# Kernel tuning notes

Measured on AMD Instinct MI355X. Metric: run time of the kernel, lower is better.

## Reference

```python
import jax, jax.numpy as jnp
import numpy as np

TEMPERATURE = 0.07
UNIFORMITY_THRESHOLD = 0.1
SEPARATION_MARGIN = 2.0
W_SUPCON = 1.0
W_SEPARATION = 0.5
W_UNIFORMITY = 0.5
NUM_MASKS = 6


def setup_inputs() -> dict:
    key = jax.random.key(0)
    k1, k2, k3 = jax.random.split(key, 3)
    B, H, Wd, D = 16, 33, 33, 512
    emb = jax.random.normal(k1, (B, H, Wd, D), dtype=jnp.float32)
    emb = emb / jnp.linalg.norm(emb, axis=-1, keepdims=True)  # module expects normalized embeddings
    masks = jax.random.uniform(k2, (B, NUM_MASKS, H, Wd), dtype=jnp.float32)
    is_forged = jax.random.uniform(k3, (B,), dtype=jnp.float32)
    return {"embeddings": emb, "masks": masks, "is_forged": is_forged}


def _labels(masks):
    # masks: (M, H, W). Channel i writes label i+1 where mask>0.5 (if channel has any mass);
    # later channels overwrite earlier -> equivalent to max over active hits.
    active = masks.sum(axis=(1, 2)) > 0  # (M,)
    hit = (masks > 0.5) & active[:, None, None]
    ids = jnp.arange(1, masks.shape[0] + 1)[:, None, None]
    return jnp.max(jnp.where(hit, ids, 0), axis=0).reshape(-1)  # (H*W,)


def _per_image(emb, masks, forged):
    H, W, D = emb.shape
    feat = emb.reshape(-1, D)  # (N, D)
    N = feat.shape[0]
    labels = _labels(masks)  # (N,) in 0..M
    L = masks.shape[0] + 1  # possible labels 0..6
    onehot = (labels[:, None] == jnp.arange(L)[None, :]).astype(feat.dtype)  # (N, L)
    cnt = onehot.sum(axis=0)  # (L,)
    sums = onehot.T @ feat  # (L, D) per-label sums
    mean_l = sums / jnp.maximum(cnt, 1.0)[:, None]  # safe per-label centroids

    # ---- SupCon (PixelSupConLoss) ----
    logits = (feat @ feat.T) / TEMPERATURE  # (N, N)
    logits = logits - jax.lax.stop_gradient(logits.max(axis=1, keepdims=True))
    same = (labels[:, None] == labels[None, :]).astype(feat.dtype)
    logits_mask = 1.0 - jnp.eye(N, dtype=feat.dtype)
    pos = same * logits_mask
    exp_l = jnp.exp(logits) * logits_mask
    log_prob = logits - jnp.log(exp_l.sum(axis=1, keepdims=True) + 1e-6)
    pos_sum = pos.sum(axis=1)
    mean_lp = (pos * log_prob).sum(axis=1) / jnp.where(pos_sum == 0, 1.0, pos_sum)
    anchor_valid = (pos_sum > 0).astype(feat.dtype)
    n_anchor = anchor_valid.sum()
    supcon = (-mean_lp * anchor_valid).sum() / jnp.maximum(n_anchor, 1.0)
    supcon_valid = n_anchor > 0

    # ---- Inter-instance separation ----
    present = cnt > 0
    cn = (mean_l ** 2).sum(axis=1)  # (L,)
    sq = cn[:, None] + cn[None, :] - 2.0 * (mean_l @ mean_l.T)  # squared centroid dists
    tri = jnp.triu(jnp.ones((L, L), dtype=bool), k=1)
    pair_valid = tri & present[:, None] & present[None, :]
    d = jnp.sqrt(jnp.where(pair_valid, jnp.maximum(sq, 0.0), 1.0))
    terms = jnp.where(pair_valid, jax.nn.relu(SEPARATION_MARGIN - d), 0.0)
    n_pairs = pair_valid.sum().astype(feat.dtype)
    sep = terms.sum() / jnp.maximum(n_pairs, 1.0)
    sep_valid = present.sum() >= 2

    # ---- Uniformity ----
    rn2 = (feat ** 2).sum(axis=1)  # (N,)
    q_l = onehot.T @ rn2  # (L,) per-label sum of squared norms
    var_l = q_l / jnp.maximum(cnt, 1.0) - (mean_l ** 2).sum(axis=1)  # E||e||^2 - ||mean||^2
    lbl_valid = (cnt >= 2) & (var_l > UNIFORMITY_THRESHOLD)
    inst_loss = jnp.where(lbl_valid, var_l - UNIFORMITY_THRESHOLD, 0.0).sum()
    n_lbl = lbl_valid.sum().astype(feat.dtype)
    uni_forged = inst_loss / jnp.maximum(n_lbl, 1.0)
    uni_forged_valid = n_lbl > 0
    mean_all = feat.mean(axis=0)
    var_all = ((feat - mean_all) ** 2).sum(axis=1).mean()
    uni_unf = jnp.where(var_all > UNIFORMITY_THRESHOLD, var_all - UNIFORMITY_THRESHOLD, 0.0)
    uni_unf_valid = var_all > UNIFORMITY_THRESHOLD

    is_f = forged >= 0.5
    uni = jnp.where(is_f, uni_forged, uni_unf)
    uni_valid = jnp.where(is_f, uni_forged_valid, uni_unf_valid)
    return supcon, supcon_valid, sep, sep_valid, uni, uni_valid


def _agg(vals, valids):
    v = valids.astype(vals.dtype)
    n = v.sum()
    return jnp.where(n > 0, (vals * v).sum() / jnp.maximum(n, 1.0), 0.0)


def reference(embeddings, masks, is_forged):
    sc, scv, sp, spv, un, unv = jax.vmap(_per_image)(embeddings, masks, is_forged)
    supcon = _agg(sc, scv)
    separation = _agg(sp, spv)
    uniformity = _agg(un, unv)
    return W_SUPCON * supcon + W_SEPARATION * separation + W_UNIFORMITY * uniformity
```

## Files before the change

### kernel.cpp

```cpp
#include <hip/hip_runtime.h>
#include <math.h>

#define NPIX 1089
#define DIM 512
#define NIMG 16
#define NLBL 8
#define NMASK 6
#define INVT 14.2857142857142857f

#define NGRP 72
#define NROWPAD 1152
#define NT9 9


typedef short v8s __attribute__((ext_vector_type(8)));
typedef float v4f __attribute__((ext_vector_type(4)));

__device__ __forceinline__ float wave_reduce(float x) {
#pragma unroll
  for (int o = 32; o > 0; o >>= 1) x += __shfl_xor(x, o, 64);
  return x;
}
__device__ __forceinline__ unsigned bfbits(float x) {
  unsigned u = __float_as_uint(x);
  return (u + 0x7FFFu + ((u >> 16) & 1u)) >> 16;
}
__device__ __forceinline__ unsigned pk(float lo, float hi) {
  return bfbits(lo) | (bfbits(hi) << 16);
}

__global__ __launch_bounds__(512) void k_packsum(const float* __restrict__ emb,
                                                 const float* __restrict__ masks,
                                                 uint2* __restrict__ bfemb2,
                                                 float* __restrict__ sums9,
                                                 int* __restrict__ labels,
                                                 float* __restrict__ cnt9,
                                                 unsigned* __restrict__ counter) {
  int b = blockIdx.y;
  int g9 = blockIdx.x >> 1, dh = blockIdx.x & 1;
  int tid = threadIdx.x, dd = tid & 63, w4 = tid >> 6, lane = tid & 63;
  __shared__ float msum[NMASK];
  __shared__ int slab[128];
  __shared__ int scnt[NLBL];
  __shared__ float4 red[8 * 8 * 64];
  if (tid < NMASK) msum[tid] = 0.f;
  if (tid < NLBL) scnt[tid] = 0;
  if (b == 0 && blockIdx.x == 0 && tid == 0) *counter = 0u;
  __syncthreads();
  {
    float am[NMASK] = {0.f, 0.f, 0.f, 0.f, 0.f, 0.f};
    for (int p = tid; p < NPIX; p += 512) {
#pragma unroll
      for (int c = 0; c < NMASK; c++) am[c] += masks[((size_t)b * NMASK + c) * NPIX + p];
    }
#pragma unroll
    for (int c = 0; c < NMASK; c++) {
      float v = wave_reduce(am[c]);
      if (lane == 0) atomicAdd(&msum[c], v);
    }
  }
  __syncthreads();
  if (tid < 128) {
    int r = g9 * 128 + tid;
    int lab = 7;
    if (r < NPIX) {
      lab = 0;
#pragma unroll
      for (int c = 0; c < NMASK; c++) {
        float mv = masks[((size_t)b * NMASK + c) * NPIX + r];
        if (mv > 0.5f && msum[c] > 0.f) lab = c + 1;
      }
    }
    slab[tid] = lab;
    if (dh == 0) {
      labels[b * NROWPAD + r] = lab;
      if (r < NPIX) atomicAdd(&scnt[lab], 1);
    }
  }
  __syncthreads();
  if (dh == 0 && tid < NLBL) cnt9[((size_t)b * NT9 + g9) * NLBL + tid] = (float)scnt[tid];
  float4 fa0 = {0,0,0,0}, fa1 = {0,0,0,0}, fa2 = {0,0,0,0}, fa3 = {0,0,0,0};
  float4 fa4 = {0,0,0,0}, fa5 = {0,0,0,0}, fa6 = {0,0,0,0}, fa7 = {0,0,0,0};
  int kc = dh * 8 + (dd >> 3), q = (dd >> 1) & 3, half = dd & 1;
#pragma unroll
  for (int k = 0; k < 16; k++) {
    int r = g9 * 128 + w4 + k * 8;
    bool v = r < NPIX;
    int rc = v ? r : (NPIX - 1);
    float4 x = ((const float4*)(emb + (size_t)(b * NPIX + rc) * DIM))[dh * 64 + dd];
    if (!v) x = make_float4(0.f, 0.f, 0.f, 0.f);
    uint2 o = make_uint2(pk(x.x, x.y), pk(x.z, x.w));
    bfemb2[((((size_t)(b * NGRP + (r >> 4)) * 16 + kc) * 64) + q * 16 + (r & 15)) * 2 + half] = o;
    int lab = __builtin_amdgcn_readfirstlane(slab[r - g9 * 128]);
    switch (lab) {
      case 0: fa0.x += x.x; fa0.y += x.y; fa0.z += x.z; fa0.w += x.w; break;
      case 1: fa1.x += x.x; fa1.y += x.y; fa1.z += x.z; fa1.w += x.w; break;
      case 2: fa2.x += x.x; fa2.y += x.y; fa2.z += x.z; fa2.w += x.w; break;
      case 3: fa3.x += x.x; fa3.y += x.y; fa3.z += x.z; fa3.w += x.w; break;
      case 4: fa4.x += x.x; fa4.y += x.y; fa4.z += x.z; fa4.w += x.w; break;
      case 5: fa5.x += x.x; fa5.y += x.y; fa5.z += x.z; fa5.w += x.w; break;
      case 6: fa6.x += x.x; fa6.y += x.y; fa6.z += x.z; fa6.w += x.w; break;
      default: fa7.x += x.x; fa7.y += x.y; fa7.z += x.z; fa7.w += x.w; break;
    }
  }
  red[(0 * 8 + w4) * 64 + dd] = fa0; red[(1 * 8 + w4) * 64 + dd] = fa1;
  red[(2 * 8 + w4) * 64 + dd] = fa2; red[(3 * 8 + w4) * 64 + dd] = fa3;
  red[(4 * 8 + w4) * 64 + dd] = fa4; red[(5 * 8 + w4) * 64 + dd] = fa5;
  red[(6 * 8 + w4) * 64 + dd] = fa6; red[(7 * 8 + w4) * 64 + dd] = fa7;
  __syncthreads();
  int l = tid >> 6, d2 = tid & 63;
  float4 s = {0,0,0,0};
#pragma unroll
  for (int ww = 0; ww < 8; ww++) {
    float4 t = red[(l * 8 + ww) * 64 + d2];
    s.x += t.x; s.y += t.y; s.z += t.z; s.w += t.w;
  }
  *(float4*)&sums9[(((size_t)(b * NT9 + g9) * NLBL + l) * DIM) + dh * 256 + d2 * 4] = s;
}

__global__ __launch_bounds__(512) void k_epass6(const uint4* __restrict__ bfemb4,
                                                float* __restrict__ E9) {
  int n = blockIdx.x;
  int img = ((n & 7) << 1) | ((n >> 3) & 1);
  int t = n >> 4;
  int it = 0, rem = t;
  while (rem >= NT9 - it) { rem -= NT9 - it; it++; }
  int jt = it + rem;
  int i0 = it * 128, j0 = jt * 128;
  bool diag = (it == jt);
  int tid = threadIdx.x, lane = tid & 63, w = tid >> 6;
  int wm = w >> 2, wn = w & 3;
  int quad = lane >> 4, l15 = lane & 15;
  __shared__ uint4 st[2][2][8][64];
  __shared__ float Ered[4][128];
  __shared__ float Ecol[2][128];

  size_t gA = ((size_t)(img * NGRP + it * 8 + w) * 16) * 64 + lane;
  size_t gB = ((size_t)(img * NGRP + jt * 8 + w) * 16) * 64 + lane;
  int bsel = diag ? 0 : 1;

#define STAGE(kc, buf)                                                          \
  {                                                                             \
    __builtin_amdgcn_global_load_lds(                                           \
        (const __attribute__((address_space(1))) void*)(bfemb4 + gA + (kc) * 64), \
        (__attribute__((address_space(3))) void*)&st[buf][0][w][0], 16, 0, 0);  \
    if (!diag)                                                                  \
      __builtin_amdgcn_global_load_lds(                                         \
          (const __attribute__((address_space(1))) void*)(bfemb4 + gB + (kc) * 64), \
          (__attribute__((address_space(3))) void*)&st[buf][1][w][0], 16, 0, 0); \
  }

  v4f acc[4][2];
#pragma unroll
  for (int mf = 0; mf < 4; mf++)
#pragma unroll
    for (int nf = 0; nf < 2; nf++) acc[mf][nf] = (v4f){0.f, 0.f, 0.f, 0.f};

  STAGE(0, 0);
  __syncthreads();
#pragma unroll
  for (int kc = 0; kc < 16; kc++) {
    int cur = kc & 1;
    if (kc < 15) STAGE(kc + 1, cur ^ 1);
    v8s a[4], b[2];
#pragma unroll
    for (int f = 0; f < 4; f++) a[f] = *(const v8s*)&st[cur][0][wm * 4 + f][lane];
#pragma unroll
    for (int f = 0; f < 2; f++) b[f] = *(const v8s*)&st[cur][bsel][wn * 2 + f][lane];
#pragma unroll
    for (int mf = 0; mf < 4; mf++)
#pragma unroll
      for (int nf = 0; nf < 2; nf++)
        acc[mf][nf] = __builtin_amdgcn_mfma_f32_16x16x32_bf16(a[mf], b[nf],
                                                              acc[mf][nf], 0, 0, 0);
    __syncthreads();
  }
#undef STAGE

  float scol[2] = {0.f, 0.f};
#pragma unroll
  for (int mf = 0; mf < 4; mf++) {
#pragma unroll
    for (int rr = 0; rr < 4; rr++) {
      int i = i0 + wm * 64 + mf * 16 + quad * 4 + rr;
      float srow = 0.f;
#pragma unroll
      for (int nf = 0; nf < 2; nf++) {
        int j = j0 + wn * 32 + nf * 16 + l15;
        float e = __expf((acc[mf][nf][rr] - 1.f) * INVT);
        bool ok = (j < NPIX) && (!diag || (i != j && i < NPIX));
        e = ok ? e : 0.f;
        srow += e;
        scol[nf] += e;
      }
      srow += __shfl_xor(srow, 1); srow += __shfl_xor(srow, 2);
      srow += __shfl_xor(srow, 4); srow += __shfl_xor(srow, 8);
      if (l15 == 0) Ered[wn][wm * 64 + mf * 16 + quad * 4 + rr] = srow;
    }
  }
  if (!diag) {
#pragma unroll
    for (int nf = 0; nf < 2; nf++) {
      float s = scol[nf];
      s += __shfl_xor(s, 16); s += __shfl_xor(s, 32);
      if (quad == 0) Ecol[wm][wn * 32 + nf * 16 + l15] = s;
    }
  }
  __syncthreads();
  if (tid < 128) {
    E9[((size_t)img * NT9 + jt) * NROWPAD + i0 + tid] =
        Ered[0][tid] + Ered[1][tid] + Ered[2][tid] + Ered[3][tid];
    if (!diag)
      E9[((size_t)img * NT9 + it) * NROWPAD + j0 + tid] = Ecol[0][tid] + Ecol[1][tid];
  }
}

__global__ __launch_bounds__(512) void k_imgfinal(const float* __restrict__ sums9,
                                                  const int* __restrict__ labels,
                                                  const float* __restrict__ cnt9,
                                                  const float* __restrict__ E9,
                                                  const float* __restrict__ is_forged,
                                                  unsigned* __restrict__ counter,
                                                  float* __restrict__ per_img,
                                                  float* __restrict__ out) {
  int b = blockIdx.x, tid = threadIdx.x;
  int wave = tid >> 6, lane = tid & 63;
  __shared__ float ssum[NLBL * DIM];
  __shared__ float sCnt[NLBL], sR[NLBL][NLBL];
  __shared__ float sLog, sNA;
  if (tid < NLBL) {
    float s = 0.f;
#pragma unroll
    for (int g = 0; g < NT9; g++) s += cnt9[((size_t)b * NT9 + g) * NLBL + tid];
    sCnt[tid] = s;
  }
  if (tid == 0) { sLog = 0.f; sNA = 0.f; }
  for (int o = tid; o < NLBL * DIM; o += 512) {
    float s = 0.f;
#pragma unroll
    for (int g = 0; g < NT9; g++) s += sums9[((size_t)(b * NT9 + g) * NLBL * DIM) + o];
    ssum[o] = s;
  }
  __syncthreads();
  float ll = 0.f, na = 0.f;
  for (int p = tid; p < NPIX; p += 512) {
    int lab = labels[b * NROWPAD + p];
    if (sCnt[lab] >= 1.5f) {
      float e = 0.f;
#pragma unroll
      for (int s = 0; s < NT9; s++) e += E9[((size_t)b * NT9 + s) * NROWPAD + p];
      ll += __logf(e + 1e-6f);
      na += 1.f;
    }
  }
  ll = wave_reduce(ll); na = wave_reduce(na);
  if (lane == 0) { atomicAdd(&sLog, ll); atomicAdd(&sNA, na); }
  for (int t = wave; t < 36; t += 8) {
    int a = 0, tt = t;
    while (tt >= NLBL - a) { tt -= NLBL - a; a++; }
    int bb = a + tt;
    float d0 = 0.f;
    for (int k = lane; k < DIM; k += 64) d0 += ssum[a * DIM + k] * ssum[bb * DIM + k];
    d0 = wave_reduce(d0);
    if (lane == 0) sR[a][bb] = d0;
  }
  __syncthreads();
  if (tid == 0) {
    float spos = 0.f;
    for (int l = 0; l < NLBL; l++) {
      float c = sCnt[l];
      if (c >= 1.5f) spos += (sR[l][l] - c) * INVT / (c - 1.f) - c * INVT;
    }
    float nA = sNA;
    float sc = nA > 0.f ? (sLog - spos) / nA : 0.f;
    float scv = nA > 0.f ? 1.f : 0.f;
    float inv[NLBL]; int present[NLBL]; int nPres = 0;
    for (int l = 0; l < NLBL; l++) {
      present[l] = sCnt[l] > 0.f;
      nPres += present[l];
      inv[l] = 1.f / fmaxf(sCnt[l], 1.f);
    }
    float sepsum = 0.f; int npairs = 0;
    for (int a = 0; a < NLBL; a++)
      for (int c = a + 1; c < NLBL; c++)
        if (present[a] && present[c]) {
          float sq_ = sR[a][a] * inv[a] * inv[a] + sR[c][c] * inv[c] * inv[c]
                    - 2.f * sR[a][c] * inv[a] * inv[c];
          float dd = sqrtf(fmaxf(sq_, 0.f));
          sepsum += fmaxf(2.f - dd, 0.f);
          npairs++;
        }
    float sep = npairs > 0 ? sepsum / (float)npairs : 0.f;
    float sepv = nPres >= 2 ? 1.f : 0.f;
    float inst = 0.f; int nlbl = 0;
    for (int l = 0; l < NLBL; l++) {
      float var = 1.f - sR[l][l] * inv[l] * inv[l];
      if (sCnt[l] >= 2.f && var > 0.1f) { inst += var - 0.1f; nlbl++; }
    }
    float unif = nlbl > 0 ? inst / (float)nlbl : 0.f;
    float unifv = nlbl > 0 ? 1.f : 0.f;
    float tot2 = 0.f;
    for (int a = 0; a < NLBL; a++) {
      tot2 += sR[a][a];
      for (int c = a + 1; c < NLBL; c++) tot2 += 2.f * sR[a][c];
    }
    float Nf = (float)NPIX;
    float var_all = 1.f - tot2 / (Nf * Nf);
    float uniu = var_all > 0.1f ? var_all - 0.1f : 0.f;
    float uniuv = var_all > 0.1f ? 1.f : 0.f;
    bool isf = is_forged[b] >= 0.5f;
    per_img[b * 6 + 0] = sc;
    per_img[b * 6 + 1] = scv;
    per_img[b * 6 + 2] = sep;
    per_img[b * 6 + 3] = sepv;
    per_img[b * 6 + 4] = isf ? unif : uniu;
    per_img[b * 6 + 5] = isf ? unifv : uniuv;
    __threadfence();
    unsigned tk = atomicAdd(counter, 1u);
    if (tk == NIMG - 1) {
      __threadfence();
      float accv[3] = {0.f, 0.f, 0.f}, accn[3] = {0.f, 0.f, 0.f};
      for (int bb = 0; bb < NIMG; bb++)
        for (int m = 0; m < 3; m++) {
          float v = per_img[bb * 6 + m * 2], val = per_img[bb * 6 + m * 2 + 1];
          accv[m] += v * val; accn[m] += val;
        }
      float scA = accn[0] > 0.f ? accv[0] / accn[0] : 0.f;
      float sepA = accn[1] > 0.f ? accv[1] / accn[1] : 0.f;
      float uniA = accn[2] > 0.f ? accv[2] / accn[2] : 0.f;
      out[0] = 1.0f * scA + 0.5f * sepA + 0.5f * uniA;
    }
  }
}

extern "C" void kernel_launch(void* const* d_in, const int* in_sizes, int n_in,
                              void* d_out, int out_size, void* d_ws, size_t ws_size,
                              hipStream_t stream) {
  const float* emb = (const float*)d_in[0];
  const float* masks = (const float*)d_in[1];
  const float* isf = (const float*)d_in[2];
  float* out = (float*)d_out;
  char* ws = (char*)d_ws;
  size_t off = 0;
  uint4* bfemb4 = (uint4*)(ws + off);
  off += (size_t)NIMG * NGRP * 16 * 64 * 16;
  float* E9 = (float*)(ws + off);     off += sizeof(float) * NIMG * NT9 * NROWPAD;
  float* sums9 = (float*)(ws + off);  off += sizeof(float) * NIMG * NT9 * NLBL * DIM;
  int* labels = (int*)(ws + off);     off += sizeof(int) * NIMG * NROWPAD;
  float* cnt9 = (float*)(ws + off);   off += sizeof(float) * NIMG * NT9 * NLBL;
  float* per_img = (float*)(ws + off); off += sizeof(float) * NIMG * 6;
  off = (off + 127) & ~(size_t)127;
  unsigned* counter = (unsigned*)(ws + off); off += 128;

  k_packsum<<<dim3(18, NIMG), 512, 0, stream>>>(emb, masks, (uint2*)bfemb4, sums9,
                                                labels, cnt9, counter);
  k_epass6<<<45 * NIMG, 512, 0, stream>>>(bfemb4, E9);
  k_imgfinal<<<NIMG, 512, 0, stream>>>(sums9, labels, cnt9, E9, isf, counter, per_img, out);
}
```

Baseline: 123.2 us.

## Fuse per-image finalization into Gram tile kernel via last-block atomic counters

Removes the separate k_imgfinal launch. Each tile block of the E-pass kernel now increments a per-image atomic counter, and the last of that image's 45 tiles runs the per-image reduction, reusing the staging LDS for label sums. A second counter picks the last image to write the scalar output. This saves a kernel launch and lets finalization of early images overlap with tiles still running for other images, at the cost of extra shared memory and a serialized tail in one block per image.

```diff
diff --git a/kernel.cpp b/kernel.cpp
--- a/kernel.cpp
+++ b/kernel.cpp
@@ -35,7 +35,7 @@
                                                  float* __restrict__ sums9,
                                                  int* __restrict__ labels,
                                                  float* __restrict__ cnt9,
-                                                 unsigned* __restrict__ counter) {
+                                                 unsigned* __restrict__ counters) {
   int b = blockIdx.y;
   int g9 = blockIdx.x >> 1, dh = blockIdx.x & 1;
   int tid = threadIdx.x, dd = tid & 63, w4 = tid >> 6, lane = tid & 63;
@@ -45,7 +45,7 @@
   __shared__ float4 red[8 * 8 * 64];
   if (tid < NMASK) msum[tid] = 0.f;
   if (tid < NLBL) scnt[tid] = 0;
-  if (b == 0 && blockIdx.x == 0 && tid == 0) *counter = 0u;
+  if (b == 0 && blockIdx.x == 0 && tid < 32) counters[tid] = 0u;
   __syncthreads();
   {
     float am[NMASK] = {0.f, 0.f, 0.f, 0.f, 0.f, 0.f};
@@ -118,8 +118,15 @@
   *(float4*)&sums9[(((size_t)(b * NT9 + g9) * NLBL + l) * DIM) + dh * 256 + d2 * 4] = s;
 }
 
-__global__ __launch_bounds__(512) void k_epass6(const uint4* __restrict__ bfemb4,
-                                                float* __restrict__ E9) {
+__global__ __launch_bounds__(512) void k_epass7(const uint4* __restrict__ bfemb4,
+                                                float* __restrict__ E9,
+                                                const float* __restrict__ sums9,
+                                                const int* __restrict__ labels,
+                                                const float* __restrict__ cnt9,
+                                                const float* __restrict__ is_forged,
+                                                unsigned* __restrict__ counters,
+                                                float* __restrict__ per_img,
+                                                float* __restrict__ out) {
   int n = blockIdx.x;
   int img = ((n & 7) << 1) | ((n >> 3) & 1);
   int t = n >> 4;
@@ -134,6 +141,9 @@
   __shared__ uint4 st[2][2][8][64];
   __shared__ float Ered[4][128];
   __shared__ float Ecol[2][128];
+  __shared__ float sCnt[NLBL], sR[NLBL][NLBL];
+  __shared__ float sLog, sNA;
+  __shared__ int sflag;
 
   size_t gA = ((size_t)(img * NGRP + it * 8 + w) * 16) * 64 + lane;
   size_t gB = ((size_t)(img * NGRP + jt * 8 + w) * 16) * 64 + lane;
@@ -213,122 +223,121 @@
     if (!diag)
       E9[((size_t)img * NT9 + it) * NROWPAD + j0 + tid] = Ecol[0][tid] + Ecol[1][tid];
   }
-}
-
-__global__ __launch_bounds__(512) void k_imgfinal(const float* __restrict__ sums9,
-                                                  const int* __restrict__ labels,
-                                                  const float* __restrict__ cnt9,
-                                                  const float* __restrict__ E9,
-                                                  const float* __restrict__ is_forged,
-                                                  unsigned* __restrict__ counter,
-                                                  float* __restrict__ per_img,
-                                                  float* __restrict__ out) {
-  int b = blockIdx.x, tid = threadIdx.x;
-  int wave = tid >> 6, lane = tid & 63;
-  __shared__ float ssum[NLBL * DIM];
-  __shared__ float sCnt[NLBL], sR[NLBL][NLBL];
-  __shared__ float sLog, sNA;
-  if (tid < NLBL) {
-    float s = 0.f;
-#pragma unroll
-    for (int g = 0; g < NT9; g++) s += cnt9[((size_t)b * NT9 + g) * NLBL + tid];
-    sCnt[tid] = s;
-  }
-  if (tid == 0) { sLog = 0.f; sNA = 0.f; }
-  for (int o = tid; o < NLBL * DIM; o += 512) {
-    float s = 0.f;
-#pragma unroll
-    for (int g = 0; g < NT9; g++) s += sums9[((size_t)(b * NT9 + g) * NLBL * DIM) + o];
-    ssum[o] = s;
-  }
-  __syncthreads();
-  float ll = 0.f, na = 0.f;
-  for (int p = tid; p < NPIX; p += 512) {
-    int lab = labels[b * NROWPAD + p];
-    if (sCnt[lab] >= 1.5f) {
-      float e = 0.f;
-#pragma unroll
-      for (int s = 0; s < NT9; s++) e += E9[((size_t)b * NT9 + s) * NROWPAD + p];
-      ll += __logf(e + 1e-6f);
-      na += 1.f;
-    }
-  }
-  ll = wave_reduce(ll); na = wave_reduce(na);
-  if (lane == 0) { atomicAdd(&sLog, ll); atomicAdd(&sNA, na); }
-  for (int t = wave; t < 36; t += 8) {
-    int a = 0, tt = t;
-    while (tt >= NLBL - a) { tt -= NLBL - a; a++; }
-    int bb = a + tt;
-    float d0 = 0.f;
-    for (int k = lane; k < DIM; k += 64) d0 += ssum[a * DIM + k] * ssum[bb * DIM + k];
-    d0 = wave_reduce(d0);
-    if (lane == 0) sR[a][bb] = d0;
-  }
   __syncthreads();
   if (tid == 0) {
-    float spos = 0.f;
-    for (int l = 0; l < NLBL; l++) {
-      float c = sCnt[l];
-      if (c >= 1.5f) spos += (sR[l][l] - c) * INVT / (c - 1.f) - c * INVT;
-    }
-    float nA = sNA;
-    float sc = nA > 0.f ? (sLog - spos) / nA : 0.f;
-    float scv = nA > 0.f ? 1.f : 0.f;
-    float inv[NLBL]; int present[NLBL]; int nPres = 0;
-    for (int l = 0; l < NLBL; l++) {
-      present[l] = sCnt[l] > 0.f;
-      nPres += present[l];
-      inv[l] = 1.f / fmaxf(sCnt[l], 1.f);
-    }
-    float sepsum = 0.f; int npairs = 0;
-    for (int a = 0; a < NLBL; a++)
-      for (int c = a + 1; c < NLBL; c++)
-        if (present[a] && present[c]) {
-          float sq_ = sR[a][a] * inv[a] * inv[a] + sR[c][c] * inv[c] * inv[c]
-                    - 2.f * sR[a][c] * inv[a] * inv[c];
-          float dd = sqrtf(fmaxf(sq_, 0.f));
-          sepsum += fmaxf(2.f - dd, 0.f);
-          npairs++;
-        }
-    float sep = npairs > 0 ? sepsum / (float)npairs : 0.f;
-    float sepv = nPres >= 2 ? 1.f : 0.f;
-    float inst = 0.f; int nlbl = 0;
-    for (int l = 0; l < NLBL; l++) {
-      float var = 1.f - sR[l][l] * inv[l] * inv[l];
-      if (sCnt[l] >= 2.f && var > 0.1f) { inst += var - 0.1f; nlbl++; }
-    }
-    float unif = nlbl > 0 ? inst / (float)nlbl : 0.f;
-    float unifv = nlbl > 0 ? 1.f : 0.f;
-    float tot2 = 0.f;
-    for (int a = 0; a < NLBL; a++) {
-      tot2 += sR[a][a];
-      for (int c = a + 1; c < NLBL; c++) tot2 += 2.f * sR[a][c];
-    }
-    float Nf = (float)NPIX;
-    float var_all = 1.f - tot2 / (Nf * Nf);
-    float uniu = var_all > 0.1f ? var_all - 0.1f : 0.f;
-    float uniuv = var_all > 0.1f ? 1.f : 0.f;
-    bool isf = is_forged[b] >= 0.5f;
-    per_img[b * 6 + 0] = sc;
-    per_img[b * 6 + 1] = scv;
-    per_img[b * 6 + 2] = sep;
-    per_img[b * 6 + 3] = sepv;
-    per_img[b * 6 + 4] = isf ? unif : uniu;
-    per_img[b * 6 + 5] = isf ? unifv : uniuv;
     __threadfence();
-    unsigned tk = atomicAdd(counter, 1u);
-    if (tk == NIMG - 1) {
+    unsigned tk = atomicAdd(&counters[img], 1u);
+    sflag = (tk == 44u) ? 1 : 0;
+  }
+  __syncthreads();
+  if (!sflag) return;
+  __threadfence();
+
+  {
+    int b = img;
+    float* ssum = (float*)&st[0][0][0][0];
+    if (tid < NLBL) {
+      float s = 0.f;
+#pragma unroll
+      for (int g = 0; g < NT9; g++) s += cnt9[((size_t)b * NT9 + g) * NLBL + tid];
+      sCnt[tid] = s;
+    }
+    if (tid == 0) { sLog = 0.f; sNA = 0.f; }
+    for (int o = tid; o < NLBL * DIM; o += 512) {
+      float s = 0.f;
+#pragma unroll
+      for (int g = 0; g < NT9; g++) s += sums9[((size_t)(b * NT9 + g) * NLBL * DIM) + o];
+      ssum[o] = s;
+    }
+    __syncthreads();
+    float ll = 0.f, na = 0.f;
+    for (int p = tid; p < NPIX; p += 512) {
+      int lab = labels[b * NROWPAD + p];
+      if (sCnt[lab] >= 1.5f) {
+        float e = 0.f;
+#pragma unroll
+        for (int s = 0; s < NT9; s++) e += E9[((size_t)b * NT9 + s) * NROWPAD + p];
+        ll += __logf(e + 1e-6f);
+        na += 1.f;
+      }
+    }
+    ll = wave_reduce(ll); na = wave_reduce(na);
+    if (lane == 0) { atomicAdd(&sLog, ll); atomicAdd(&sNA, na); }
+    for (int tp = w; tp < 36; tp += 8) {
+      int a = 0, tt = tp;
+      while (tt >= NLBL - a) { tt -= NLBL - a; a++; }
+      int bb = a + tt;
+      float d0 = 0.f;
+      for (int k = lane; k < DIM; k += 64) d0 += ssum[a * DIM + k] * ssum[bb * DIM + k];
+      d0 = wave_reduce(d0);
+      if (lane == 0) sR[a][bb] = d0;
+    }
+    __syncthreads();
+    if (tid == 0) {
+      float spos = 0.f;
+      for (int l = 0; l < NLBL; l++) {
+        float c = sCnt[l];
+        if (c >= 1.5f) spos += (sR[l][l] - c) * INVT / (c - 1.f) - c * INVT;
+      }
+      float nA = sNA;
+      float sc = nA > 0.f ? (sLog - spos) / nA : 0.f;
+      float scv = nA > 0.f ? 1.f : 0.f;
+      float inv[NLBL]; int present[NLBL]; int nPres = 0;
+      for (int l = 0; l < NLBL; l++) {
+        present[l] = sCnt[l] > 0.f;
+        nPres += present[l];
+        inv[l] = 1.f / fmaxf(sCnt[l], 1.f);
+      }
+      float sepsum = 0.f; int npairs = 0;
+      for (int a = 0; a < NLBL; a++)
+        for (int c = a + 1; c < NLBL; c++)
+          if (present[a] && present[c]) {
+            float sq_ = sR[a][a] * inv[a] * inv[a] + sR[c][c] * inv[c] * inv[c]
+                      - 2.f * sR[a][c] * inv[a] * inv[c];
+            float dd = sqrtf(fmaxf(sq_, 0.f));
+            sepsum += fmaxf(2.f - dd, 0.f);
+            npairs++;
+          }
+      float sep = npairs > 0 ? sepsum / (float)npairs : 0.f;
+      float sepv = nPres >= 2 ? 1.f : 0.f;
+      float inst = 0.f; int nlbl = 0;
+      for (int l = 0; l < NLBL; l++) {
+        float var = 1.f - sR[l][l] * inv[l] * inv[l];
+        if (sCnt[l] >= 2.f && var > 0.1f) { inst += var - 0.1f; nlbl++; }
+      }
+      float unif = nlbl > 0 ? inst / (float)nlbl : 0.f;
+      float unifv = nlbl > 0 ? 1.f : 0.f;
+      float tot2 = 0.f;
+      for (int a = 0; a < NLBL; a++) {
+        tot2 += sR[a][a];
+        for (int c = a + 1; c < NLBL; c++) tot2 += 2.f * sR[a][c];
+      }
+      float Nf = (float)NPIX;
+      float var_all = 1.f - tot2 / (Nf * Nf);
+      float uniu = var_all > 0.1f ? var_all - 0.1f : 0.f;
+      float uniuv = var_all > 0.1f ? 1.f : 0.f;
+      bool isf = is_forged[b] >= 0.5f;
+      per_img[b * 6 + 0] = sc;
+      per_img[b * 6 + 1] = scv;
+      per_img[b * 6 + 2] = sep;
+      per_img[b * 6 + 3] = sepv;
+      per_img[b * 6 + 4] = isf ? unif : uniu;
+      per_img[b * 6 + 5] = isf ? unifv : uniuv;
       __threadfence();
-      float accv[3] = {0.f, 0.f, 0.f}, accn[3] = {0.f, 0.f, 0.f};
-      for (int bb = 0; bb < NIMG; bb++)
-        for (int m = 0; m < 3; m++) {
-          float v = per_img[bb * 6 + m * 2], val = per_img[bb * 6 + m * 2 + 1];
-          accv[m] += v * val; accn[m] += val;
-        }
-      float scA = accn[0] > 0.f ? accv[0] / accn[0] : 0.f;
-      float sepA = accn[1] > 0.f ? accv[1] / accn[1] : 0.f;
-      float uniA = accn[2] > 0.f ? accv[2] / accn[2] : 0.f;
-      out[0] = 1.0f * scA + 0.5f * sepA + 0.5f * uniA;
+      unsigned tk2 = atomicAdd(&counters[16], 1u);
+      if (tk2 == NIMG - 1) {
+        __threadfence();
+        float accv[3] = {0.f, 0.f, 0.f}, accn[3] = {0.f, 0.f, 0.f};
+        for (int bb = 0; bb < NIMG; bb++)
+          for (int m = 0; m < 3; m++) {
+            float v = per_img[bb * 6 + m * 2], val = per_img[bb * 6 + m * 2 + 1];
+            accv[m] += v * val; accn[m] += val;
+          }
+        float scA = accn[0] > 0.f ? accv[0] / accn[0] : 0.f;
+        float sepA = accn[1] > 0.f ? accv[1] / accn[1] : 0.f;
+        float uniA = accn[2] > 0.f ? accv[2] / accn[2] : 0.f;
+        out[0] = 1.0f * scA + 0.5f * sepA + 0.5f * uniA;
+      }
     }
   }
 }
@@ -350,10 +359,10 @@
   float* cnt9 = (float*)(ws + off);   off += sizeof(float) * NIMG * NT9 * NLBL;
   float* per_img = (float*)(ws + off); off += sizeof(float) * NIMG * 6;
   off = (off + 127) & ~(size_t)127;
-  unsigned* counter = (unsigned*)(ws + off); off += 128;
+  unsigned* counters = (unsigned*)(ws + off); off += 128;
 
   k_packsum<<<dim3(18, NIMG), 512, 0, stream>>>(emb, masks, (uint2*)bfemb4, sums9,
-                                                labels, cnt9, counter);
-  k_epass6<<<45 * NIMG, 512, 0, stream>>>(bfemb4, E9);
-  k_imgfinal<<<NIMG, 512, 0, stream>>>(sums9, labels, cnt9, E9, isf, counter, per_img, out);
-}
+                                                labels, cnt9, counters);
+  k_epass7<<<45 * NIMG, 512, 0, stream>>>(bfemb4, E9, sums9, labels, cnt9, isf,
+                                          counters, per_img, out);
+}
```

Result: slower. 140.3 us (+13.8%).

## Triple-buffer Gram-tile K loop with explicit vmcnt waits and single barrier

Applied to the files above, without the earlier changes.

Replaces the double-buffered K loop in the Gram/exp kernel with a three-stage LDS ring. Loads run two chunks ahead, and each iteration does one partial s_waitcnt vmcnt plus one barrier instead of a full __syncthreads pair. The loop is specialised for diagonal tiles (one load per stage) and off-diagonal tiles (two loads per stage) so the vmcnt count is right for each. The aim is to hide global-to-LDS latency behind MFMA work, at the cost of more LDS per block. The last two iterations issue harmless wrap-around loads.

```diff
diff --git a/kernel.cpp b/kernel.cpp
--- a/kernel.cpp
+++ b/kernel.cpp
@@ -118,7 +118,7 @@
   *(float4*)&sums9[(((size_t)(b * NT9 + g9) * NLBL + l) * DIM) + dh * 256 + d2 * 4] = s;
 }
 
-__global__ __launch_bounds__(512) void k_epass6(const uint4* __restrict__ bfemb4,
+__global__ __launch_bounds__(512) void k_epass8(const uint4* __restrict__ bfemb4,
                                                 float* __restrict__ E9) {
   int n = blockIdx.x;
   int img = ((n & 7) << 1) | ((n >> 3) & 1);
@@ -131,7 +131,7 @@
   int tid = threadIdx.x, lane = tid & 63, w = tid >> 6;
   int wm = w >> 2, wn = w & 3;
   int quad = lane >> 4, l15 = lane & 15;
-  __shared__ uint4 st[2][2][8][64];
+  __shared__ uint4 st[3][2][8][64];
   __shared__ float Ered[4][128];
   __shared__ float Ecol[2][128];
 
@@ -150,6 +150,24 @@
           (__attribute__((address_space(3))) void*)&st[buf][1][w][0], 16, 0, 0); \
   }
 
+#define KLOOP(VMC)                                                              \
+  _Pragma("unroll")                                                             \
+  for (int kc = 0; kc < 16; kc++) {                                             \
+    asm volatile("s_waitcnt vmcnt(" #VMC ")" ::: "memory");                     \
+    __builtin_amdgcn_s_barrier();                                               \
+    __builtin_amdgcn_sched_barrier(0);                                          \
+    STAGE((kc + 2) & 15, (kc + 2) % 3);                                         \
+    v8s a[4], b[2];                                                             \
+    _Pragma("unroll") for (int f = 0; f < 4; f++)                               \
+        a[f] = *(const v8s*)&st[kc % 3][0][wm * 4 + f][lane];                   \
+    _Pragma("unroll") for (int f = 0; f < 2; f++)                               \
+        b[f] = *(const v8s*)&st[kc % 3][bsel][wn * 2 + f][lane];                \
+    _Pragma("unroll") for (int mf = 0; mf < 4; mf++)                            \
+        _Pragma("unroll") for (int nf = 0; nf < 2; nf++)                        \
+            acc[mf][nf] = __builtin_amdgcn_mfma_f32_16x16x32_bf16(              \
+                a[mf], b[nf], acc[mf][nf], 0, 0, 0);                            \
+  }
+
   v4f acc[4][2];
 #pragma unroll
   for (int mf = 0; mf < 4; mf++)
@@ -157,24 +175,13 @@
     for (int nf = 0; nf < 2; nf++) acc[mf][nf] = (v4f){0.f, 0.f, 0.f, 0.f};
 
   STAGE(0, 0);
-  __syncthreads();
-#pragma unroll
-  for (int kc = 0; kc < 16; kc++) {
-    int cur = kc & 1;
-    if (kc < 15) STAGE(kc + 1, cur ^ 1);
-    v8s a[4], b[2];
-#pragma unroll
-    for (int f = 0; f < 4; f++) a[f] = *(const v8s*)&st[cur][0][wm * 4 + f][lane];
-#pragma unroll
-    for (int f = 0; f < 2; f++) b[f] = *(const v8s*)&st[cur][bsel][wn * 2 + f][lane];
-#pragma unroll
-    for (int mf = 0; mf < 4; mf++)
-#pragma unroll
-      for (int nf = 0; nf < 2; nf++)
-        acc[mf][nf] = __builtin_amdgcn_mfma_f32_16x16x32_bf16(a[mf], b[nf],
-                                                              acc[mf][nf], 0, 0, 0);
-    __syncthreads();
-  }
+  STAGE(1, 1);
+  if (!diag) {
+    KLOOP(2)
+  } else {
+    KLOOP(1)
+  }
+#undef KLOOP
 #undef STAGE
 
   float scol[2] = {0.f, 0.f};
@@ -354,6 +361,6 @@
 
   k_packsum<<<dim3(18, NIMG), 512, 0, stream>>>(emb, masks, (uint2*)bfemb4, sums9,
                                                 labels, cnt9, counter);
-  k_epass6<<<45 * NIMG, 512, 0, stream>>>(bfemb4, E9);
+  k_epass8<<<45 * NIMG, 512, 0, stream>>>(bfemb4, E9);
   k_imgfinal<<<NIMG, 512, 0, stream>>>(sums9, labels, cnt9, E9, isf, counter, per_img, out);
 }
```

Result: slower. 125.9 us (+2.2%).
